# Performance work log

Measured on AMD Instinct MI355X. Metric: run time of the kernel, lower is better.

The kernel has to match this reference:

```python
import jax, jax.numpy as jnp
import numpy as np
from jax import lax

B, C, D, H, W = 2, 32, 64, 128, 128
TAU = 0.1          # temperature
P_CAP = 2048       # max_pos_per_image
NEG_CAP = int(6.0 * 2048)  # neg_pos_ratio * max_pos (static padding cap)
KS = 11            # dilation_kernel_size
EPS = 1e-8
NEG_INF = -1e9


def setup_inputs() -> dict:
    key = jax.random.key(0)
    features = jax.random.normal(key, (B, C, D, H, W), dtype=jnp.float32)
    # Foreground box: 10x12x12 = 1440 voxels per image (< P_CAP, so no
    # random subsampling happens in the original torch module either).
    lab = np.zeros((B, D, H, W), dtype=np.int32)
    lab[:, 20:30, 40:52, 40:52] = 1
    return {"features": features, "labels": jnp.asarray(lab)}


def _dilate(fg):
    """Binary dilation of (B,D,H,W) bool mask via max-pool, SAME padding."""
    p = KS // 2
    x = lax.reduce_window(fg.astype(jnp.float32), 0.0, lax.max,
                          (1, KS, KS, KS), (1, 1, 1, 1),
                          [(0, 0), (p, p), (p, p), (p, p)])
    return x > 0


def _image_loss(feat, fg, rim):
    """feat: (N,C) L2-normalized; fg, rim: (N,) bool. Returns (loss, valid)."""
    # Deterministic 'first-index' selection into fixed-size padded slots
    # (stable argsort puts True-mask pixels first, in ascending index order).
    pos_idx = jnp.argsort(jnp.logical_not(fg))[:P_CAP]
    pos_valid = fg[pos_idx]                      # (P_CAP,)
    neg_idx = jnp.argsort(jnp.logical_not(rim))[:NEG_CAP]
    neg_valid = rim[neg_idx]                     # (NEG_CAP,)

    pos_f = feat[pos_idx]                        # (P_CAP, C)
    neg_f = feat[neg_idx]                        # (NEG_CAP, C)

    pp = jnp.einsum('ic,jc->ij', pos_f, pos_f) / TAU   # (P_CAP, P_CAP)
    pn = jnp.einsum('ic,kc->ik', pos_f, neg_f) / TAU   # (P_CAP, NEG_CAP)

    eye = jnp.eye(P_CAP, dtype=bool)
    pos_col = pos_valid[None, :] & ~eye          # valid positive columns (no self)
    pp = jnp.where(pos_col, pp, NEG_INF)         # diag -> -1e9 (as in torch)
    pn = jnp.where(neg_valid[None, :], pn, NEG_INF)

    all_logits = jnp.concatenate([pp, pn], axis=1)
    m = jnp.max(all_logits, axis=1, keepdims=True)
    exp_all = jnp.exp(all_logits - m)            # padded cols underflow to 0
    numerator = jnp.sum(exp_all[:, :P_CAP] * pos_col, axis=1) + EPS
    denominator = jnp.sum(exp_all, axis=1) + EPS
    loss_i = -jnp.log(numerator / denominator)

    anchor_valid = pos_valid & (numerator > EPS)
    cnt = jnp.sum(anchor_valid.astype(jnp.float32))
    img_loss = jnp.sum(loss_i * anchor_valid) / jnp.maximum(cnt, 1.0)

    n_pos = jnp.sum(fg)
    n_rim = jnp.sum(rim)
    img_valid = (n_pos >= 2) & (n_rim > 0) & jnp.any(anchor_valid)
    return img_loss, img_valid


def _forward(features, labels):
    b, c = features.shape[0], features.shape[1]
    feats = features.reshape(b, c, -1)                       # (B,C,N)
    nrm = jnp.sqrt(jnp.sum(feats * feats, axis=1, keepdims=True))
    feats = feats / jnp.maximum(nrm, 1e-12)                  # F.normalize, dim=1
    feats = jnp.transpose(feats, (0, 2, 1))                  # (B,N,C)

    fg = labels > 0                                          # (B,D,H,W)
    rim = _dilate(fg) & ~fg
    fg_flat = fg.reshape(b, -1)
    rim_flat = rim.reshape(b, -1)

    losses, valids = jax.vmap(_image_loss)(feats, fg_flat, rim_flat)
    vf = valids.astype(jnp.float32)
    total = jnp.sum(losses * vf) / jnp.maximum(jnp.sum(vf), 1.0)
    return jnp.where(jnp.any(valids), total, jnp.float32(0.0))


def reference(features, labels):
    return _forward(features, labels)
```

## Files before the change

kernel.cpp:

```cpp
#include <hip/hip_runtime.h>
#include <math.h>

#define B_ 2
#define C_ 32
#define D_ 64
#define H_ 128
#define W_ 128
#define N_ (D_*H_*W_)
#define NW_ (N_/64)
#define P_CAP 2048
#define NEG_CAP 12288
#define PAD 5
#define EPS_ 1e-8f
#define SLICES 64
#define TA 4

__global__ __launch_bounds__(256) void k_packW(const int* __restrict__ labels,
                                               unsigned long long* __restrict__ fgbits,
                                               unsigned long long* __restrict__ dilw,
                                               int* cnt_pos, int* cnt_neg,
                                               float* loss_sum, float* acnt) {
    if (blockIdx.x == 0 && threadIdx.x < B_) {
        int t = threadIdx.x;
        cnt_pos[t] = 0; cnt_neg[t] = 0; loss_sum[t] = 0.f; acnt[t] = 0.f;
    }
    const int g = blockIdx.x * 256 + threadIdx.x;
    const int lane = threadIdx.x & 63;
    const int w = threadIdx.x >> 6;
    const int word = (blockIdx.x << 2) + w;

    unsigned long long fgw = __ballot(labels[g] > 0);
    __shared__ unsigned long long smem[4];
    if (lane == 0) { fgbits[word] = fgw; smem[w] = fgw; }
    __syncthreads();
    unsigned long long self = smem[w];
    unsigned long long other = smem[w ^ 1];
    unsigned long long out = self;
    if ((word & 1) == 0) {
#pragma unroll
        for (int k = 1; k <= PAD; ++k)
            out |= (self >> k) | (self << k) | (other << (64 - k));
    } else {
#pragma unroll
        for (int k = 1; k <= PAD; ++k)
            out |= (self << k) | (self >> k) | (other >> (64 - k));
    }
    if (lane == 0) dilw[word] = out;
}

__global__ __launch_bounds__(256) void k_dilH(const unsigned long long* __restrict__ in,
                                              unsigned long long* __restrict__ out) {
    const int q = blockIdx.x * 256 + threadIdx.x;
    const int qq = q & (NW_ - 1);
    const int h = (qq >> 1) & (H_ - 1);
    const int lo = (h >= PAD) ? -PAD : -h;
    const int hi = (h + PAD <= H_ - 1) ? PAD : (H_ - 1 - h);
    unsigned long long v = 0;
    for (int o = lo; o <= hi; ++o) v |= in[q + o * 2];
    out[q] = v;
}

__global__ __launch_bounds__(256) void k_dilD(const unsigned long long* __restrict__ in,
                                              unsigned long long* __restrict__ out) {
    const int q = blockIdx.x * 256 + threadIdx.x;
    const int qq = q & (NW_ - 1);
    const int d = qq >> 8;
    const int lo = (d >= PAD) ? -PAD : -d;
    const int hi = (d + PAD <= D_ - 1) ? PAD : (D_ - 1 - d);
    unsigned long long v = 0;
    for (int o = lo; o <= hi; ++o) v |= in[q + o * (H_ * 2)];
    out[q] = v;
}

__global__ __launch_bounds__(256) void k_cg(const float* __restrict__ features,
                                            const unsigned long long* __restrict__ fgbits,
                                            const unsigned long long* __restrict__ dild,
                                            int* cnt_pos, int* cnt_neg,
                                            float* __restrict__ pos_feat,
                                            float* __restrict__ neg_feat) {
    const int g = blockIdx.x * 256 + threadIdx.x;
    const int lane = threadIdx.x & 63;
    const int word = g >> 6;
    const int b = g >> 20;
    const int n = g & (N_ - 1);

    unsigned long long fgw = fgbits[word];
    unsigned long long rimw = dild[word] & ~fgw;
    if ((fgw | rimw) == 0) return;

    int basep = 0, basen = 0;
    if (lane == 0) {
        if (fgw)  basep = atomicAdd(&cnt_pos[b], __popcll(fgw));
        if (rimw) basen = atomicAdd(&cnt_neg[b], __popcll(rimw));
    }
    basep = __shfl(basep, 0);
    basen = __shfl(basen, 0);

    const unsigned long long ltmask = (lane == 0) ? 0ull : (~0ull >> (64 - lane));
    const bool is_fg = (fgw >> lane) & 1;
    const bool is_rim = (rimw >> lane) & 1;
    if (!is_fg && !is_rim) return;

    int slot; float* dst;
    if (is_fg) {
        slot = basep + __popcll(fgw & ltmask);
        if (slot >= P_CAP) return;
        dst = pos_feat + ((size_t)b * P_CAP + slot) * C_;
    } else {
        slot = basen + __popcll(rimw & ltmask);
        if (slot >= NEG_CAP) return;
        dst = neg_feat + ((size_t)b * NEG_CAP + slot) * C_;
    }

    const float* fbase = features + (size_t)b * C_ * N_ + n;
    float v[C_];
    float ss = 0.f;
#pragma unroll
    for (int c = 0; c < C_; ++c) {
        float x = fbase[(size_t)c * N_];
        v[c] = x;
        ss += x * x;
    }
    float inv = 1.0f / fmaxf(sqrtf(ss), 1e-12f);
#pragma unroll
    for (int c = 0; c < C_; ++c) dst[c] = v[c] * inv;
}

__device__ __forceinline__ void dot4x(const float4* __restrict__ row4,
                                      const float A[TA][C_], float d[TA]) {
    d[0] = d[1] = d[2] = d[3] = 0.f;
#pragma unroll
    for (int q = 0; q < 8; ++q) {
        float4 v = row4[q];
#pragma unroll
        for (int i = 0; i < TA; ++i) {
            d[i] = fmaf(v.x, A[i][4*q+0], d[i]);
            d[i] = fmaf(v.y, A[i][4*q+1], d[i]);
            d[i] = fmaf(v.z, A[i][4*q+2], d[i]);
            d[i] = fmaf(v.w, A[i][4*q+3], d[i]);
        }
    }
}

__global__ __launch_bounds__(256, 3) void k_loss2(const float* __restrict__ pos_feat,
                                                  const float* __restrict__ neg_feat,
                                                  const int* __restrict__ cnt_pos,
                                                  const int* __restrict__ cnt_neg,
                                                  float* __restrict__ partial) {
    const int slice = blockIdx.x;
    const int tile  = blockIdx.y;
    const int b     = blockIdx.z;
    const int np = min(cnt_pos[b], P_CAP);
    const int nn = min(cnt_neg[b], NEG_CAP);
    const int abase = tile * 256;
    if (abase >= np) return;
    const int total = np + nn;
    const int tid = threadIdx.x;
    const int lane = tid & 63;
    const int w = __builtin_amdgcn_readfirstlane(tid >> 6);

    __shared__ float4 sA4[256 * 8];
    {
        const float4* src = (const float4*)(pos_feat + ((size_t)b * P_CAP + abase) * C_);
#pragma unroll
        for (int k = 0; k < 8; ++k) {
            const int idx = tid + k * 256;
            const int r = idx >> 3, q = idx & 7;
            sA4[(r << 3) | ((q + r) & 7)] = src[idx];
        }
    }
    __syncthreads();

    float A[TA][C_];
#pragma unroll
    for (int i = 0; i < TA; ++i) {
        const int r = i * 64 + lane;
        const int rbase = r << 3;
        const int rot = r & 7;
#pragma unroll
        for (int q = 0; q < 8; ++q) {
            float4 v = sA4[rbase | ((q + rot) & 7)];
            A[i][4*q+0] = v.x; A[i][4*q+1] = v.y; A[i][4*q+2] = v.z; A[i][4*q+3] = v.w;
        }
    }
    __syncthreads();

    float ps[TA] = {0.f, 0.f, 0.f, 0.f};
    float ns[TA] = {0.f, 0.f, 0.f, 0.f};

    const int per = (total + SLICES - 1) / SLICES;
    const int r0 = slice * per;
    const int r1 = min(r0 + per, total);
    const int a1 = abase + lane;

    const int pEnd = min(r1, np);
    const float4* pbase4 = (const float4*)(pos_feat + (size_t)b * P_CAP * C_);
    for (int gr = r0 + w; gr < pEnd; gr += 4) {
        float d[TA];
        dot4x(pbase4 + gr * 8, A, d);
#pragma unroll
        for (int i = 0; i < TA; ++i) {
            float e = __expf(fmaf(d[i], 10.f, -10.f));
            ps[i] += (gr == a1 + 64 * i) ? 0.f : e;
        }
    }
    const int s0 = max(r0, np);
    const float4* nbase4 = (const float4*)(neg_feat + (size_t)b * NEG_CAP * C_);
    for (int gr = s0 + w; gr < r1; gr += 4) {
        float d[TA];
        dot4x(nbase4 + (gr - np) * 8, A, d);
#pragma unroll
        for (int i = 0; i < TA; ++i)
            ns[i] += __expf(fmaf(d[i], 10.f, -10.f));
    }

    float* redP = (float*)sA4;
    float* redN = (float*)sA4 + 4 * 256;
#pragma unroll
    for (int i = 0; i < TA; ++i) {
        redP[w * 256 + i * 64 + lane] = ps[i];
        redN[w * 256 + i * 64 + lane] = ns[i];
    }
    __syncthreads();
    {
        float p = redP[0*256 + tid] + redP[1*256 + tid] + redP[2*256 + tid] + redP[3*256 + tid];
        float n = redN[0*256 + tid] + redN[1*256 + tid] + redN[2*256 + tid] + redN[3*256 + tid];
        float* dst = partial + ((size_t)(b * SLICES + slice) * 2) * P_CAP;
        dst[abase + tid] = p;
        dst[P_CAP + abase + tid] = n;
    }
}

__global__ __launch_bounds__(256) void k_loss_fin(const float* __restrict__ partial,
                                                  const int* __restrict__ cnt_pos,
                                                  float* __restrict__ loss_sum,
                                                  float* __restrict__ acnt) {
    const int blocks_per_b = P_CAP / 256;
    const int b = blockIdx.x / blocks_per_b;
    const int a = (blockIdx.x % blocks_per_b) * 256 + threadIdx.x;
    const int np = min(cnt_pos[b], P_CAP);
    const int tid = threadIdx.x;
    float loss = 0.f, cnt = 0.f;
    if (a < np) {
        float num = 0.f, den = 0.f;
        for (int s = 0; s < SLICES; ++s) {
            const float* base = partial + ((size_t)(b * SLICES + s) * 2) * P_CAP;
            num += base[a];
            den += base[P_CAP + a];
        }
        if (num > 0.f) {
            den += num;
            num += EPS_; den += EPS_;
            loss = __logf(den) - __logf(num);
            cnt = 1.f;
        }
    }
    __shared__ float sl[256], sc[256];
    sl[tid] = loss; sc[tid] = cnt;
    __syncthreads();
    for (int off = 128; off > 0; off >>= 1) {
        if (tid < off) { sl[tid] += sl[tid + off]; sc[tid] += sc[tid + off]; }
        __syncthreads();
    }
    if (tid == 0 && sc[0] > 0.f) {
        atomicAdd(&loss_sum[b], sl[0]);
        atomicAdd(&acnt[b], sc[0]);
    }
}

__global__ void k_final(const int* cnt_pos, const int* cnt_neg,
                        const float* loss_sum, const float* acnt, float* out) {
    float tot = 0.f, nv = 0.f;
    bool any = false;
    for (int b = 0; b < B_; ++b) {
        bool valid = (cnt_pos[b] >= 2) && (cnt_neg[b] > 0) && (acnt[b] > 0.f);
        float il = loss_sum[b] / fmaxf(acnt[b], 1.f);
        if (valid) { tot += il; nv += 1.f; any = true; }
    }
    out[0] = any ? tot / fmaxf(nv, 1.f) : 0.f;
}

extern "C" void kernel_launch(void* const* d_in, const int* in_sizes, int n_in,
                              void* d_out, int out_size, void* d_ws, size_t ws_size,
                              hipStream_t stream) {
    const float* features = (const float*)d_in[0];
    const int* labels = (const int*)d_in[1];
    float* out = (float*)d_out;

    char* p = (char*)d_ws;
    float* pos_feat = (float*)p;                 p += (size_t)B_ * P_CAP * C_ * 4;
    float* neg_feat = (float*)p;                 p += (size_t)B_ * NEG_CAP * C_ * 4;
    float* partial = (float*)p;                  p += (size_t)B_ * SLICES * 2 * P_CAP * 4;
    unsigned long long* fgbits = (unsigned long long*)p;  p += (size_t)B_ * NW_ * 8;
    unsigned long long* dilw = (unsigned long long*)p;    p += (size_t)B_ * NW_ * 8;
    unsigned long long* dilh = (unsigned long long*)p;    p += (size_t)B_ * NW_ * 8;
    unsigned long long* dild = (unsigned long long*)p;    p += (size_t)B_ * NW_ * 8;
    int* cnt_pos = (int*)p;                      p += B_ * 4;
    int* cnt_neg = (int*)p;                      p += B_ * 4;
    float* loss_sum = (float*)p;                 p += B_ * 4;
    float* acnt = (float*)p;                     p += B_ * 4;

    const int threads = 256;
    const int vox_blocks = B_ * N_ / threads;
    const int word_blocks = B_ * NW_ / threads;

    k_packW<<<vox_blocks, threads, 0, stream>>>(labels, fgbits, dilw,
                                                cnt_pos, cnt_neg, loss_sum, acnt);
    k_dilH<<<word_blocks, threads, 0, stream>>>(dilw, dilh);
    k_dilD<<<word_blocks, threads, 0, stream>>>(dilh, dild);
    k_cg<<<vox_blocks, threads, 0, stream>>>(features, fgbits, dild,
                                             cnt_pos, cnt_neg, pos_feat, neg_feat);
    dim3 lgrid(SLICES, P_CAP / 256, B_);
    k_loss2<<<lgrid, 256, 0, stream>>>(pos_feat, neg_feat, cnt_pos, cnt_neg, partial);
    k_loss_fin<<<B_ * (P_CAP / 256), 256, 0, stream>>>(partial, cnt_pos, loss_sum, acnt);
    k_final<<<1, 1, 0, stream>>>(cnt_pos, cnt_neg, loss_sum, acnt, out);
}
```

Before: 371.1 us.

## Fuse dilation passes with compaction, stage candidate rows in LDS, fold final reduce

Merges the H and D dilation kernels and the compaction/gather kernel into one per-(b,d) block kernel that ORs the dilated words directly from the W-dilated bitmask and then walks 64 words per wave. This removes two intermediate bitmask buffers and two launches. The loss kernel now cooperatively stages chunks of positive/negative rows into shared memory before the dot products, instead of having each wave read rows from global memory. The final scalar reduction is folded into the fin kernel via a last-block atomic counter. The trade-offs are serial per-wave loops with lower parallelism in the gather, and added shared memory that may reduce loss-kernel occupancy.

```diff
diff --git a/kernel.cpp b/kernel.cpp
--- a/kernel.cpp
+++ b/kernel.cpp
@@ -14,20 +14,24 @@
 #define EPS_ 1e-8f
 #define SLICES 64
 #define TA 4
+#define CHUNK 160
 
 __global__ __launch_bounds__(256) void k_packW(const int* __restrict__ labels,
                                                unsigned long long* __restrict__ fgbits,
                                                unsigned long long* __restrict__ dilw,
                                                int* cnt_pos, int* cnt_neg,
-                                               float* loss_sum, float* acnt) {
-    if (blockIdx.x == 0 && threadIdx.x < B_) {
-        int t = threadIdx.x;
-        cnt_pos[t] = 0; cnt_neg[t] = 0; loss_sum[t] = 0.f; acnt[t] = 0.f;
-    }
-    const int g = blockIdx.x * 256 + threadIdx.x;
+                                               float* loss_sum, float* acnt, int* done_cnt) {
+    if (blockIdx.x == 0) {
+        if (threadIdx.x < B_) {
+            int t = threadIdx.x;
+            cnt_pos[t] = 0; cnt_neg[t] = 0; loss_sum[t] = 0.f; acnt[t] = 0.f;
+        }
+        if (threadIdx.x == 64) *done_cnt = 0;
+    }
     const int lane = threadIdx.x & 63;
     const int w = threadIdx.x >> 6;
     const int word = (blockIdx.x << 2) + w;
+    const int g = blockIdx.x * 256 + threadIdx.x;
 
     unsigned long long fgw = __ballot(labels[g] > 0);
     __shared__ unsigned long long smem[4];
@@ -48,82 +52,80 @@
     if (lane == 0) dilw[word] = out;
 }
 
-__global__ __launch_bounds__(256) void k_dilH(const unsigned long long* __restrict__ in,
-                                              unsigned long long* __restrict__ out) {
-    const int q = blockIdx.x * 256 + threadIdx.x;
-    const int qq = q & (NW_ - 1);
-    const int h = (qq >> 1) & (H_ - 1);
-    const int lo = (h >= PAD) ? -PAD : -h;
-    const int hi = (h + PAD <= H_ - 1) ? PAD : (H_ - 1 - h);
+__global__ __launch_bounds__(256) void k_maskCG(const float* __restrict__ features,
+                                                const unsigned long long* __restrict__ fgbits,
+                                                const unsigned long long* __restrict__ dilw,
+                                                int* cnt_pos, int* cnt_neg,
+                                                float* __restrict__ pos_feat,
+                                                float* __restrict__ neg_feat) {
+    const int bd = blockIdx.x;
+    const int b = bd >> 6;
+    const int d = bd & 63;
+    const int tid = threadIdx.x;
+    const int h = tid >> 1;
+
+    const int qbase = b * NW_ + d * 256;
+    const int q = qbase + tid;
+    const int dlo = (d >= PAD) ? -PAD : -d;
+    const int dhi = (d + PAD <= D_ - 1) ? PAD : (D_ - 1 - d);
+    const int hlo = (h >= PAD) ? -PAD : -h;
+    const int hhi = (h + PAD <= H_ - 1) ? PAD : (H_ - 1 - h);
     unsigned long long v = 0;
-    for (int o = lo; o <= hi; ++o) v |= in[q + o * 2];
-    out[q] = v;
-}
-
-__global__ __launch_bounds__(256) void k_dilD(const unsigned long long* __restrict__ in,
-                                              unsigned long long* __restrict__ out) {
-    const int q = blockIdx.x * 256 + threadIdx.x;
-    const int qq = q & (NW_ - 1);
-    const int d = qq >> 8;
-    const int lo = (d >= PAD) ? -PAD : -d;
-    const int hi = (d + PAD <= D_ - 1) ? PAD : (D_ - 1 - d);
-    unsigned long long v = 0;
-    for (int o = lo; o <= hi; ++o) v |= in[q + o * (H_ * 2)];
-    out[q] = v;
-}
-
-__global__ __launch_bounds__(256) void k_cg(const float* __restrict__ features,
-                                            const unsigned long long* __restrict__ fgbits,
-                                            const unsigned long long* __restrict__ dild,
-                                            int* cnt_pos, int* cnt_neg,
-                                            float* __restrict__ pos_feat,
-                                            float* __restrict__ neg_feat) {
-    const int g = blockIdx.x * 256 + threadIdx.x;
-    const int lane = threadIdx.x & 63;
-    const int word = g >> 6;
-    const int b = g >> 20;
-    const int n = g & (N_ - 1);
-
-    unsigned long long fgw = fgbits[word];
-    unsigned long long rimw = dild[word] & ~fgw;
-    if ((fgw | rimw) == 0) return;
-
-    int basep = 0, basen = 0;
-    if (lane == 0) {
-        if (fgw)  basep = atomicAdd(&cnt_pos[b], __popcll(fgw));
-        if (rimw) basen = atomicAdd(&cnt_neg[b], __popcll(rimw));
-    }
-    basep = __shfl(basep, 0);
-    basen = __shfl(basen, 0);
-
+    for (int od = dlo; od <= dhi; ++od)
+        for (int oh = hlo; oh <= hhi; ++oh)
+            v |= dilw[q + od * 256 + oh * 2];
+
+    __shared__ unsigned long long sDil[256];
+    __shared__ unsigned long long sFg[256];
+    sFg[tid] = fgbits[q];
+    sDil[tid] = v;
+    __syncthreads();
+
+    const int lane = tid & 63;
+    const int w = tid >> 6;
     const unsigned long long ltmask = (lane == 0) ? 0ull : (~0ull >> (64 - lane));
-    const bool is_fg = (fgw >> lane) & 1;
-    const bool is_rim = (rimw >> lane) & 1;
-    if (!is_fg && !is_rim) return;
-
-    int slot; float* dst;
-    if (is_fg) {
-        slot = basep + __popcll(fgw & ltmask);
-        if (slot >= P_CAP) return;
-        dst = pos_feat + ((size_t)b * P_CAP + slot) * C_;
-    } else {
-        slot = basen + __popcll(rimw & ltmask);
-        if (slot >= NEG_CAP) return;
-        dst = neg_feat + ((size_t)b * NEG_CAP + slot) * C_;
-    }
-
-    const float* fbase = features + (size_t)b * C_ * N_ + n;
-    float v[C_];
-    float ss = 0.f;
-#pragma unroll
-    for (int c = 0; c < C_; ++c) {
-        float x = fbase[(size_t)c * N_];
-        v[c] = x;
-        ss += x * x;
-    }
-    float inv = 1.0f / fmaxf(sqrtf(ss), 1e-12f);
-#pragma unroll
-    for (int c = 0; c < C_; ++c) dst[c] = v[c] * inv;
+    for (int k = 0; k < 64; ++k) {
+        const int widx = w * 64 + k;
+        const unsigned long long fgw = sFg[widx];
+        const unsigned long long rimw = sDil[widx] & ~fgw;
+        if ((fgw | rimw) == 0) continue;
+
+        int basep = 0, basen = 0;
+        if (lane == 0) {
+            if (fgw)  basep = atomicAdd(&cnt_pos[b], __popcll(fgw));
+            if (rimw) basen = atomicAdd(&cnt_neg[b], __popcll(rimw));
+        }
+        basep = __shfl(basep, 0);
+        basen = __shfl(basen, 0);
+
+        const bool is_fg = (fgw >> lane) & 1;
+        const bool is_rim = (rimw >> lane) & 1;
+        if (is_fg || is_rim) {
+            const int n = (((d << 8) | widx) << 6) | lane;
+            int slot; float* dst = nullptr;
+            if (is_fg) {
+                slot = basep + __popcll(fgw & ltmask);
+                if (slot < P_CAP) dst = pos_feat + ((size_t)b * P_CAP + slot) * C_;
+            } else {
+                slot = basen + __popcll(rimw & ltmask);
+                if (slot < NEG_CAP) dst = neg_feat + ((size_t)b * NEG_CAP + slot) * C_;
+            }
+            if (dst) {
+                const float* fbase = features + (size_t)b * C_ * N_ + n;
+                float vv[C_];
+                float ss = 0.f;
+#pragma unroll
+                for (int c = 0; c < C_; ++c) {
+                    float x = fbase[(size_t)c * N_];
+                    vv[c] = x;
+                    ss += x * x;
+                }
+                float inv = 1.0f / fmaxf(sqrtf(ss), 1e-12f);
+#pragma unroll
+                for (int c = 0; c < C_; ++c) dst[c] = vv[c] * inv;
+            }
+        }
+    }
 }
 
 __device__ __forceinline__ void dot4x(const float4* __restrict__ row4,
@@ -160,6 +162,8 @@
     const int w = __builtin_amdgcn_readfirstlane(tid >> 6);
 
     __shared__ float4 sA4[256 * 8];
+    __shared__ float4 sP[CHUNK * 8];
+
     {
         const float4* src = (const float4*)(pos_feat + ((size_t)b * P_CAP + abase) * C_);
 #pragma unroll
@@ -183,7 +187,6 @@
             A[i][4*q+0] = v.x; A[i][4*q+1] = v.y; A[i][4*q+2] = v.z; A[i][4*q+3] = v.w;
         }
     }
-    __syncthreads();
 
     float ps[TA] = {0.f, 0.f, 0.f, 0.f};
     float ns[TA] = {0.f, 0.f, 0.f, 0.f};
@@ -193,27 +196,38 @@
     const int r1 = min(r0 + per, total);
     const int a1 = abase + lane;
 
-    const int pEnd = min(r1, np);
     const float4* pbase4 = (const float4*)(pos_feat + (size_t)b * P_CAP * C_);
-    for (int gr = r0 + w; gr < pEnd; gr += 4) {
-        float d[TA];
-        dot4x(pbase4 + gr * 8, A, d);
-#pragma unroll
-        for (int i = 0; i < TA; ++i) {
-            float e = __expf(fmaf(d[i], 10.f, -10.f));
-            ps[i] += (gr == a1 + 64 * i) ? 0.f : e;
-        }
-    }
-    const int s0 = max(r0, np);
     const float4* nbase4 = (const float4*)(neg_feat + (size_t)b * NEG_CAP * C_);
-    for (int gr = s0 + w; gr < r1; gr += 4) {
-        float d[TA];
-        dot4x(nbase4 + (gr - np) * 8, A, d);
-#pragma unroll
-        for (int i = 0; i < TA; ++i)
-            ns[i] += __expf(fmaf(d[i], 10.f, -10.f));
-    }
-
+
+    for (int c0 = r0; c0 < r1; c0 += CHUNK) {
+        const int cnt = min(CHUNK, r1 - c0);
+        __syncthreads();
+        for (int idx = tid; idx < cnt * 8; idx += 256) {
+            const int r = idx >> 3, q = idx & 7;
+            const int gr = c0 + r;
+            sP[idx] = (gr < np) ? pbase4[gr * 8 + q] : nbase4[(size_t)(gr - np) * 8 + q];
+        }
+        __syncthreads();
+#pragma unroll 2
+        for (int r = w; r < cnt; r += 4) {
+            const int gr = c0 + r;
+            float dv[TA];
+            dot4x(&sP[r * 8], A, dv);
+            if (gr < np) {
+#pragma unroll
+                for (int i = 0; i < TA; ++i) {
+                    float e = __expf(fmaf(dv[i], 10.f, -10.f));
+                    ps[i] += (gr == a1 + 64 * i) ? 0.f : e;
+                }
+            } else {
+#pragma unroll
+                for (int i = 0; i < TA; ++i)
+                    ns[i] += __expf(fmaf(dv[i], 10.f, -10.f));
+            }
+        }
+    }
+
+    __syncthreads();
     float* redP = (float*)sA4;
     float* redN = (float*)sA4 + 4 * 256;
 #pragma unroll
@@ -231,10 +245,14 @@
     }
 }
 
-__global__ __launch_bounds__(256) void k_loss_fin(const float* __restrict__ partial,
-                                                  const int* __restrict__ cnt_pos,
-                                                  float* __restrict__ loss_sum,
-                                                  float* __restrict__ acnt) {
+#define FIN_BLOCKS (B_ * (P_CAP / 256))
+__global__ __launch_bounds__(256) void k_fin(const float* __restrict__ partial,
+                                             const int* __restrict__ cnt_pos,
+                                             const int* __restrict__ cnt_neg,
+                                             float* __restrict__ loss_sum,
+                                             float* __restrict__ acnt,
+                                             int* __restrict__ done_cnt,
+                                             float* __restrict__ out) {
     const int blocks_per_b = P_CAP / 256;
     const int b = blockIdx.x / blocks_per_b;
     const int a = (blockIdx.x % blocks_per_b) * 256 + threadIdx.x;
@@ -262,22 +280,26 @@
         if (tid < off) { sl[tid] += sl[tid + off]; sc[tid] += sc[tid + off]; }
         __syncthreads();
     }
-    if (tid == 0 && sc[0] > 0.f) {
-        atomicAdd(&loss_sum[b], sl[0]);
-        atomicAdd(&acnt[b], sc[0]);
-    }
-}
-
-__global__ void k_final(const int* cnt_pos, const int* cnt_neg,
-                        const float* loss_sum, const float* acnt, float* out) {
-    float tot = 0.f, nv = 0.f;
-    bool any = false;
-    for (int b = 0; b < B_; ++b) {
-        bool valid = (cnt_pos[b] >= 2) && (cnt_neg[b] > 0) && (acnt[b] > 0.f);
-        float il = loss_sum[b] / fmaxf(acnt[b], 1.f);
-        if (valid) { tot += il; nv += 1.f; any = true; }
-    }
-    out[0] = any ? tot / fmaxf(nv, 1.f) : 0.f;
+    if (tid == 0) {
+        if (sc[0] > 0.f) {
+            atomicAdd(&loss_sum[b], sl[0]);
+            atomicAdd(&acnt[b], sc[0]);
+        }
+        __threadfence();
+        int done = atomicAdd(done_cnt, 1);
+        if (done == FIN_BLOCKS - 1) {
+            float tot = 0.f, nv = 0.f;
+            bool any = false;
+            for (int bb = 0; bb < B_; ++bb) {
+                float ls = atomicAdd(&loss_sum[bb], 0.f);
+                float ac = atomicAdd(&acnt[bb], 0.f);
+                bool valid = (cnt_pos[bb] >= 2) && (cnt_neg[bb] > 0) && (ac > 0.f);
+                float il = ls / fmaxf(ac, 1.f);
+                if (valid) { tot += il; nv += 1.f; any = true; }
+            }
+            out[0] = any ? tot / fmaxf(nv, 1.f) : 0.f;
+        }
+    }
 }
 
 extern "C" void kernel_launch(void* const* d_in, const int* in_sizes, int n_in,
@@ -293,25 +315,21 @@
     float* partial = (float*)p;                  p += (size_t)B_ * SLICES * 2 * P_CAP * 4;
     unsigned long long* fgbits = (unsigned long long*)p;  p += (size_t)B_ * NW_ * 8;
     unsigned long long* dilw = (unsigned long long*)p;    p += (size_t)B_ * NW_ * 8;
-    unsigned long long* dilh = (unsigned long long*)p;    p += (size_t)B_ * NW_ * 8;
-    unsigned long long* dild = (unsigned long long*)p;    p += (size_t)B_ * NW_ * 8;
     int* cnt_pos = (int*)p;                      p += B_ * 4;
     int* cnt_neg = (int*)p;                      p += B_ * 4;
     float* loss_sum = (float*)p;                 p += B_ * 4;
     float* acnt = (float*)p;                     p += B_ * 4;
+    int* done_cnt = (int*)p;                     p += 4;
 
     const int threads = 256;
     const int vox_blocks = B_ * N_ / threads;
-    const int word_blocks = B_ * NW_ / threads;
 
     k_packW<<<vox_blocks, threads, 0, stream>>>(labels, fgbits, dilw,
-                                                cnt_pos, cnt_neg, loss_sum, acnt);
-    k_dilH<<<word_blocks, threads, 0, stream>>>(dilw, dilh);
-    k_dilD<<<word_blocks, threads, 0, stream>>>(dilh, dild);
-    k_cg<<<vox_blocks, threads, 0, stream>>>(features, fgbits, dild,
-                                             cnt_pos, cnt_neg, pos_feat, neg_feat);
+                                                cnt_pos, cnt_neg, loss_sum, acnt, done_cnt);
+    k_maskCG<<<B_ * D_, threads, 0, stream>>>(features, fgbits, dilw,
+                                              cnt_pos, cnt_neg, pos_feat, neg_feat);
     dim3 lgrid(SLICES, P_CAP / 256, B_);
     k_loss2<<<lgrid, 256, 0, stream>>>(pos_feat, neg_feat, cnt_pos, cnt_neg, partial);
-    k_loss_fin<<<B_ * (P_CAP / 256), 256, 0, stream>>>(partial, cnt_pos, loss_sum, acnt);
-    k_final<<<1, 1, 0, stream>>>(cnt_pos, cnt_neg, loss_sum, acnt, out);
-}
+    k_fin<<<FIN_BLOCKS, 256, 0, stream>>>(partial, cnt_pos, cnt_neg,
+                                          loss_sum, acnt, done_cnt, out);
+}
```

New measurement: 418.9 us. 1.13x slower.
